# Optimization experiments

Hardware: AMD Instinct MI355X
Metric: run time of the kernel (lower is better)

The kernel has to match this reference:

```python
import jax, jax.numpy as jnp
import numpy as np

N_NODES = 100000
N_EDGES = 3200000
FEATURE = 128
HIDDEN = 128
N_LAYERS = 3


def _glorot(key, fan_in, fan_out):
    lim = np.sqrt(6.0 / (fan_in + fan_out)).astype(np.float32)
    return jax.random.uniform(key, (fan_in, fan_out), jnp.float32, -lim, lim)


def setup_inputs() -> dict:
    key = jax.random.key(0)
    ks = jax.random.split(key, 8)
    x = jax.random.normal(ks[0], (N_NODES, FEATURE), jnp.float32)
    edge_index = jax.random.randint(ks[1], (2, N_EDGES), 0, N_NODES, jnp.int64)
    W0 = _glorot(ks[2], FEATURE, HIDDEN)
    W1 = _glorot(ks[3], HIDDEN, HIDDEN)
    W2 = _glorot(ks[4], HIDDEN, HIDDEN)
    b0 = jnp.zeros((HIDDEN,), jnp.float32)
    b1 = jnp.zeros((HIDDEN,), jnp.float32)
    b2 = jnp.zeros((HIDDEN,), jnp.float32)
    return {"x": x, "edge_index": edge_index,
            "W0": W0, "b0": b0, "W1": W1, "b1": b1, "W2": W2, "b2": b2}


def _gcn_conv(x, W, b, src, dst, n):
    # PyG GCNConv: linear -> add self loops -> sym-norm aggregate -> +bias
    h = x @ W  # [N, H]
    loop = jnp.arange(n)
    s = jnp.concatenate([src, loop])  # sources incl. self loops
    d = jnp.concatenate([dst, loop])  # targets incl. self loops
    deg = jax.ops.segment_sum(jnp.ones_like(d, dtype=h.dtype), d, num_segments=n)
    dinv = jnp.where(deg > 0, jax.lax.rsqrt(jnp.maximum(deg, 1.0)), 0.0)
    norm = dinv[s] * dinv[d]  # [E+N]
    out = jax.ops.segment_sum(h[s] * norm[:, None], d, num_segments=n)
    return out + b


def reference(x, edge_index, W0, b0, W1, b1, W2, b2):
    # forward of GCN: (GCNConv -> relu -> dropout[eval=no-op]) x layer
    src, dst = edge_index[0], edge_index[1]
    n = x.shape[0]
    for W, b in ((W0, b0), (W1, b1), (W2, b2)):
        x = jax.nn.relu(_gcn_conv(x, W, b, src, dst, n))
    return x
```

## Files before the change

kernel.cpp:

```cpp
#include <hip/hip_runtime.h>
#include <hip/hip_fp16.h>

#define N_NODES 100000
#define N_EDGES 3200000
#define NBUCKETS 391
#define CHUNK 12500


__global__ __launch_bounds__(512) void k_bzero(int* __restrict__ bucket_cnt) {
    int t = threadIdx.x;
    if (t < NBUCKETS) bucket_cnt[t] = 0;
}

__global__ __launch_bounds__(256) void k_bhist(const int* __restrict__ ei_dst,
                                               int* __restrict__ bucket_cnt) {
    __shared__ int h[NBUCKETS];
    int t = threadIdx.x;
    for (int i = t; i < NBUCKETS; i += 256) h[i] = 0;
    __syncthreads();
    int base = blockIdx.x * CHUNK;
    for (int i = t; i < CHUNK; i += 256)
        atomicAdd(&h[ei_dst[base + i] >> 8], 1);
    __syncthreads();
    for (int i = t; i < NBUCKETS; i += 256)
        if (h[i]) atomicAdd(&bucket_cnt[i], h[i]);
}

__global__ __launch_bounds__(512) void k_bscan(const int* __restrict__ bucket_cnt,
                                               int* __restrict__ bucket_base,
                                               int* __restrict__ bucket_fill) {
    __shared__ int s[512];
    int t = threadIdx.x;
    int v = (t < NBUCKETS) ? bucket_cnt[t] : 0;
    s[t] = v;
    __syncthreads();
    for (int off = 1; off < 512; off <<= 1) {
        int x = (t >= off) ? s[t - off] : 0;
        __syncthreads();
        s[t] += x;
        __syncthreads();
    }
    int ex = s[t] - v;
    if (t < NBUCKETS) { bucket_base[t] = ex; bucket_fill[t] = ex; }
    if (t == NBUCKETS - 1) bucket_base[NBUCKETS] = s[t];
}

__global__ __launch_bounds__(256) void k_bscatter(const int* __restrict__ ei,
                                                  int* __restrict__ bucket_fill,
                                                  unsigned* __restrict__ bpairs) {
    __shared__ int h[NBUCKETS];
    __shared__ int basep[NBUCKETS];
    int t = threadIdx.x;
    const int* dstp = ei + N_EDGES;
    int base = blockIdx.x * CHUNK;

    for (int i = t; i < NBUCKETS; i += 256) h[i] = 0;
    __syncthreads();
    for (int i = t; i < CHUNK; i += 256)
        atomicAdd(&h[dstp[base + i] >> 8], 1);
    __syncthreads();
    for (int i = t; i < NBUCKETS; i += 256) {
        int c = h[i];
        basep[i] = c ? atomicAdd(&bucket_fill[i], c) : 0;
    }
    __syncthreads();
    for (int i = t; i < NBUCKETS; i += 256) h[i] = 0;
    __syncthreads();
    for (int i = t; i < CHUNK; i += 256) {
        int d = dstp[base + i];
        int s = ei[base + i];
        int b = d >> 8;
        int r = atomicAdd(&h[b], 1);
        bpairs[basep[b] + r] = (unsigned)s | ((unsigned)(d & 255) << 17);
    }
}

__global__ __launch_bounds__(256) void k_bbuild(const unsigned* __restrict__ bpairs,
                                                const int* __restrict__ bucket_base,
                                                int* __restrict__ row_ptr,
                                                int* __restrict__ cnt,
                                                float* __restrict__ dinv,
                                                int* __restrict__ csr_src) {
    __shared__ int h[256];
    __shared__ int sc[256];
    int b = blockIdx.x;
    int t = threadIdx.x;
    int e0 = bucket_base[b], e1 = bucket_base[b + 1];

    h[t] = 0;
    __syncthreads();
    for (int i = e0 + t; i < e1; i += 256)
        atomicAdd(&h[bpairs[i] >> 17], 1);
    __syncthreads();
    int v = h[t];
    sc[t] = v;
    __syncthreads();
    for (int off = 1; off < 256; off <<= 1) {
        int x = (t >= off) ? sc[t - off] : 0;
        __syncthreads();
        sc[t] += x;
        __syncthreads();
    }
    int ex = sc[t] - v;
    int node = b * 256 + t;
    if (node < N_NODES) {
        cnt[node] = v;
        dinv[node] = rsqrtf((float)(v + 1));
        row_ptr[node] = e0 + ex;
    }
    __syncthreads();
    h[t] = e0 + ex;
    __syncthreads();
    for (int i = e0 + t; i < e1; i += 256) {
        unsigned p = bpairs[i];
        int pos = atomicAdd(&h[p >> 17], 1);
        csr_src[pos] = (int)(p & 0x1FFFFu);
    }
}


__global__ __launch_bounds__(256) void k_gemm(const float* __restrict__ X,
                                              const float* __restrict__ W,
                                              const float* __restrict__ dinv,
                                              __half* __restrict__ H16) {
    __shared__ float Ws[64 * 128];
    __shared__ float Xs[64 * 65];

    int t  = threadIdx.x;
    int row0 = blockIdx.x * 64;
    int cg = (t & 15) << 3;
    int rg = (t >> 4) << 2;

    float acc[4][8];
#pragma unroll
    for (int i = 0; i < 4; ++i)
#pragma unroll
        for (int j = 0; j < 8; ++j) acc[i][j] = 0.0f;

    int srow = t >> 4;
    int sk4  = (t & 15) << 2;

    for (int p = 0; p < 2; ++p) {
        __syncthreads();
        const float4* W4 = (const float4*)(W + p * 64 * 128);
        for (int i = t; i < 2048; i += 256) {
            float4 wv = W4[i];
            float* q = &Ws[i << 2];
            q[0] = wv.x; q[1] = wv.y; q[2] = wv.z; q[3] = wv.w;
        }
#pragma unroll
        for (int it = 0; it < 4; ++it) {
            int r = srow + (it << 4);
            int grow = row0 + r;
            if (grow >= N_NODES) grow = N_NODES - 1;
            float4 xv = *(const float4*)(X + (long long)grow * 128 + p * 64 + sk4);
            float* q = &Xs[r * 65 + sk4];
            q[0] = xv.x; q[1] = xv.y; q[2] = xv.z; q[3] = xv.w;
        }
        __syncthreads();
#pragma unroll
        for (int k = 0; k < 64; ++k) {
            const float4 w0 = *(const float4*)&Ws[k * 128 + cg];
            const float4 w1 = *(const float4*)&Ws[k * 128 + cg + 4];
            float x0 = Xs[(rg + 0) * 65 + k];
            float x1 = Xs[(rg + 1) * 65 + k];
            float x2 = Xs[(rg + 2) * 65 + k];
            float x3 = Xs[(rg + 3) * 65 + k];
            acc[0][0] += x0 * w0.x; acc[0][1] += x0 * w0.y; acc[0][2] += x0 * w0.z; acc[0][3] += x0 * w0.w;
            acc[0][4] += x0 * w1.x; acc[0][5] += x0 * w1.y; acc[0][6] += x0 * w1.z; acc[0][7] += x0 * w1.w;
            acc[1][0] += x1 * w0.x; acc[1][1] += x1 * w0.y; acc[1][2] += x1 * w0.z; acc[1][3] += x1 * w0.w;
            acc[1][4] += x1 * w1.x; acc[1][5] += x1 * w1.y; acc[1][6] += x1 * w1.z; acc[1][7] += x1 * w1.w;
            acc[2][0] += x2 * w0.x; acc[2][1] += x2 * w0.y; acc[2][2] += x2 * w0.z; acc[2][3] += x2 * w0.w;
            acc[2][4] += x2 * w1.x; acc[2][5] += x2 * w1.y; acc[2][6] += x2 * w1.z; acc[2][7] += x2 * w1.w;
            acc[3][0] += x3 * w0.x; acc[3][1] += x3 * w0.y; acc[3][2] += x3 * w0.z; acc[3][3] += x3 * w0.w;
            acc[3][4] += x3 * w1.x; acc[3][5] += x3 * w1.y; acc[3][6] += x3 * w1.z; acc[3][7] += x3 * w1.w;
        }
    }

#pragma unroll
    for (int i = 0; i < 4; ++i) {
        int grow = row0 + rg + i;
        if (grow >= N_NODES) break;
        float sc = dinv[grow];
        float4 pack;
        __half2* ph = (__half2*)&pack;
        ph[0] = __floats2half2_rn(acc[i][0] * sc, acc[i][1] * sc);
        ph[1] = __floats2half2_rn(acc[i][2] * sc, acc[i][3] * sc);
        ph[2] = __floats2half2_rn(acc[i][4] * sc, acc[i][5] * sc);
        ph[3] = __floats2half2_rn(acc[i][6] * sc, acc[i][7] * sc);
        *(float4*)(H16 + (long long)grow * 128 + cg) = pack;
    }
}


__global__ __launch_bounds__(256) void k_gather(const __half2* __restrict__ H2,
                                                const int* __restrict__ csr_src,
                                                const int* __restrict__ row_ptr,
                                                const int* __restrict__ cnt,
                                                const float* __restrict__ dinv,
                                                const float* __restrict__ b,
                                                float* __restrict__ out) {
    int node = blockIdx.x * 4 + (threadIdx.x >> 6);
    int lane = threadIdx.x & 63;
    if (node >= N_NODES) return;

    int start = row_ptr[node];
    int n = cnt[node];

    float2 self_ = __half22float2(H2[node * 64 + lane]);
    float accx = self_.x, accy = self_.y;

    int j = 0;
    for (; j + 8 <= n; j += 8) {
        int s[8];
#pragma unroll
        for (int u = 0; u < 8; ++u) s[u] = csr_src[start + j + u];
        float2 h[8];
#pragma unroll
        for (int u = 0; u < 8; ++u) h[u] = __half22float2(H2[s[u] * 64 + lane]);
#pragma unroll
        for (int u = 0; u < 8; ++u) { accx += h[u].x; accy += h[u].y; }
    }
    for (; j < n; ++j) {
        float2 h = __half22float2(H2[csr_src[start + j] * 64 + lane]);
        accx += h.x; accy += h.y;
    }

    float dd = dinv[node];
    float2 bb = ((const float2*)b)[lane];
    float2 v;
    v.x = fmaxf(fmaf(accx, dd, bb.x), 0.0f);
    v.y = fmaxf(fmaf(accy, dd, bb.y), 0.0f);
    ((float2*)out)[node * 64 + lane] = v;
}


extern "C" void kernel_launch(void* const* d_in, const int* in_sizes, int n_in,
                              void* d_out, int out_size, void* d_ws, size_t ws_size,
                              hipStream_t stream) {
    const float* x  = (const float*)d_in[0];
    const int*   ei = (const int*)d_in[1];
    const float* Wm[3] = {(const float*)d_in[2], (const float*)d_in[4], (const float*)d_in[6]};
    const float* bv[3] = {(const float*)d_in[3], (const float*)d_in[5], (const float*)d_in[7]};
    float* out = (float*)d_out;

    char* w = (char*)d_ws;
    int*      row_ptr     = (int*)(w + 0);
    int*      cnt         = (int*)(w + 400384);
    float*    dinv        = (float*)(w + 800768);
    int*      bucket_cnt  = (int*)(w + 1201152);
    int*      bucket_base = (int*)(w + 1203200);
    int*      bucket_fill = (int*)(w + 1205248);
    unsigned* bpairs      = (unsigned*)(w + 1207296);
    int*      csr_src     = (int*)(w + 14007808);
    __half*   H16         = (__half*)(w + 26808320);

    k_bzero<<<1, 512, 0, stream>>>(bucket_cnt);
    k_bhist<<<256, 256, 0, stream>>>(ei + N_EDGES, bucket_cnt);
    k_bscan<<<1, 512, 0, stream>>>(bucket_cnt, bucket_base, bucket_fill);
    k_bscatter<<<256, 256, 0, stream>>>(ei, bucket_fill, bpairs);
    k_bbuild<<<NBUCKETS, 256, 0, stream>>>(bpairs, bucket_base, row_ptr, cnt, dinv, csr_src);

    const float* xin = x;
    for (int l = 0; l < 3; ++l) {
        k_gemm<<<(N_NODES + 63) / 64, 256, 0, stream>>>(xin, Wm[l], dinv, H16);
        k_gather<<<(N_NODES + 3) / 4, 256, 0, stream>>>((const __half2*)H16, csr_src,
                                                        row_ptr, cnt, dinv, bv[l], out);
        xin = out;
    }
}
```

Before: 705.4 us.

## Replace FP32 SIMT GEMM with split-bf16 MFMA GEMM and pre-swizzled weight fragments

Replaces the shared-memory FP32 FMA GEMM with a matrix-core kernel using bf16 16x16x32 MFMA. FP32 accuracy is approximated with a three-term hi/lo split (hi*hi + lo*hi + hi*lo). A new prep kernel converts all three weight matrices once into fragment-ordered bf16 hi/lo arrays. Activations are loaded straight from global memory into registers and split per element, with no LDS staging. The costs are three times the MFMA count plus per-element split arithmetic, and the epilogue now writes scattered 2-byte stores instead of 16-byte vector stores.

New measurement: 650.6 us. 7.8% less time.

```diff
diff --git a/kernel.cpp b/kernel.cpp
--- a/kernel.cpp
+++ b/kernel.cpp
@@ -5,6 +5,19 @@
 #define N_EDGES 3200000
 #define NBUCKETS 391
 #define CHUNK 12500
+
+typedef __attribute__((ext_vector_type(8))) short sh8;
+typedef __attribute__((ext_vector_type(4))) float fl4;
+
+__device__ inline void split_bf16(float x, short& hi, short& lo) {
+    unsigned u = __float_as_uint(x);
+    unsigned r = u + 0x7FFFu + ((u >> 16) & 1u);
+    hi = (short)(r >> 16);
+    float hif = __uint_as_float(r & 0xFFFF0000u);
+    float lof = x - hif;
+    unsigned u2 = __float_as_uint(lof);
+    lo = (short)((u2 + 0x7FFFu + ((u2 >> 16) & 1u)) >> 16);
+}
 
 
 __global__ __launch_bounds__(512) void k_bzero(int* __restrict__ bucket_cnt) {
@@ -119,77 +132,97 @@
 }
 
 
-__global__ __launch_bounds__(256) void k_gemm(const float* __restrict__ X,
-                                              const float* __restrict__ W,
-                                              const float* __restrict__ dinv,
-                                              __half* __restrict__ H16) {
-    __shared__ float Ws[64 * 128];
-    __shared__ float Xs[64 * 65];
-
-    int t  = threadIdx.x;
-    int row0 = blockIdx.x * 64;
-    int cg = (t & 15) << 3;
-    int rg = (t >> 4) << 2;
-
-    float acc[4][8];
-#pragma unroll
-    for (int i = 0; i < 4; ++i)
-#pragma unroll
-        for (int j = 0; j < 8; ++j) acc[i][j] = 0.0f;
-
-    int srow = t >> 4;
-    int sk4  = (t & 15) << 2;
-
-    for (int p = 0; p < 2; ++p) {
-        __syncthreads();
-        const float4* W4 = (const float4*)(W + p * 64 * 128);
-        for (int i = t; i < 2048; i += 256) {
-            float4 wv = W4[i];
-            float* q = &Ws[i << 2];
-            q[0] = wv.x; q[1] = wv.y; q[2] = wv.z; q[3] = wv.w;
+__global__ __launch_bounds__(256) void k_wprep(const float* __restrict__ W0,
+                                               const float* __restrict__ W1,
+                                               const float* __restrict__ W2,
+                                               short* __restrict__ fhi,
+                                               short* __restrict__ flo) {
+    int idx = blockIdx.x * 256 + threadIdx.x;
+    int l = idx >> 14, e = idx & 16383;
+    const float* W = (l == 0) ? W0 : (l == 1) ? W1 : W2;
+    float w = W[e];
+    int k = e >> 7, n = e & 127;
+    int ks = k >> 5, q = (k >> 3) & 3, j = k & 7;
+    int c = n >> 4, n16 = n & 15;
+    int lane = q * 16 + n16;
+    int dst = ((l * 32 + ks * 8 + c) * 64 + lane) * 8 + j;
+    short hi, lo;
+    split_bf16(w, hi, lo);
+    fhi[dst] = hi;
+    flo[dst] = lo;
+}
+
+
+__global__ __launch_bounds__(256) void k_gemm_mfma(const float* __restrict__ X,
+                                                   const short* __restrict__ fhi,
+                                                   const short* __restrict__ flo,
+                                                   const float* __restrict__ dinv,
+                                                   __half* __restrict__ H16,
+                                                   int layer) {
+    int t = threadIdx.x;
+    int wave = t >> 6, lane = t & 63;
+    int q = lane >> 4, n16 = lane & 15;
+    int row_base = blockIdx.x * 128 + wave * 32;
+
+    const sh8* __restrict__ BH = (const sh8*)(fhi + layer * 16384);
+    const sh8* __restrict__ BL = (const sh8*)(flo + layer * 16384);
+
+    fl4 acc[2][8];
+#pragma unroll
+    for (int r = 0; r < 2; ++r)
+#pragma unroll
+        for (int c = 0; c < 8; ++c) acc[r][c] = (fl4){0.f, 0.f, 0.f, 0.f};
+
+    long long arow[2];
+    {
+        int r0 = row_base + n16;       if (r0 > N_NODES - 1) r0 = N_NODES - 1;
+        int r1 = row_base + 16 + n16;  if (r1 > N_NODES - 1) r1 = N_NODES - 1;
+        arow[0] = r0; arow[1] = r1;
+    }
+
+#pragma unroll
+    for (int ks = 0; ks < 4; ++ks) {
+        sh8 ah[2], al[2];
+#pragma unroll
+        for (int r = 0; r < 2; ++r) {
+            const float* px = X + arow[r] * 128 + ks * 32 + q * 8;
+            float4 x0 = *(const float4*)px;
+            float4 x1 = *(const float4*)(px + 4);
+            float xs[8] = {x0.x, x0.y, x0.z, x0.w, x1.x, x1.y, x1.z, x1.w};
+#pragma unroll
+            for (int j = 0; j < 8; ++j) {
+                short h, l;
+                split_bf16(xs[j], h, l);
+                ah[r][j] = h;
+                al[r][j] = l;
+            }
         }
 #pragma unroll
-        for (int it = 0; it < 4; ++it) {
-            int r = srow + (it << 4);
-            int grow = row0 + r;
-            if (grow >= N_NODES) grow = N_NODES - 1;
-            float4 xv = *(const float4*)(X + (long long)grow * 128 + p * 64 + sk4);
-            float* q = &Xs[r * 65 + sk4];
-            q[0] = xv.x; q[1] = xv.y; q[2] = xv.z; q[3] = xv.w;
+        for (int c = 0; c < 8; ++c) {
+            sh8 bh = BH[(ks * 8 + c) * 64 + lane];
+            sh8 bl = BL[(ks * 8 + c) * 64 + lane];
+#pragma unroll
+            for (int r = 0; r < 2; ++r) {
+                acc[r][c] = __builtin_amdgcn_mfma_f32_16x16x32_bf16(ah[r], bh, acc[r][c], 0, 0, 0);
+                acc[r][c] = __builtin_amdgcn_mfma_f32_16x16x32_bf16(al[r], bh, acc[r][c], 0, 0, 0);
+                acc[r][c] = __builtin_amdgcn_mfma_f32_16x16x32_bf16(ah[r], bl, acc[r][c], 0, 0, 0);
+            }
         }
-        __syncthreads();
-#pragma unroll
-        for (int k = 0; k < 64; ++k) {
-            const float4 w0 = *(const float4*)&Ws[k * 128 + cg];
-            const float4 w1 = *(const float4*)&Ws[k * 128 + cg + 4];
-            float x0 = Xs[(rg + 0) * 65 + k];
-            float x1 = Xs[(rg + 1) * 65 + k];
-            float x2 = Xs[(rg + 2) * 65 + k];
-            float x3 = Xs[(rg + 3) * 65 + k];
-            acc[0][0] += x0 * w0.x; acc[0][1] += x0 * w0.y; acc[0][2] += x0 * w0.z; acc[0][3] += x0 * w0.w;
-            acc[0][4] += x0 * w1.x; acc[0][5] += x0 * w1.y; acc[0][6] += x0 * w1.z; acc[0][7] += x0 * w1.w;
-            acc[1][0] += x1 * w0.x; acc[1][1] += x1 * w0.y; acc[1][2] += x1 * w0.z; acc[1][3] += x1 * w0.w;
-            acc[1][4] += x1 * w1.x; acc[1][5] += x1 * w1.y; acc[1][6] += x1 * w1.z; acc[1][7] += x1 * w1.w;
-            acc[2][0] += x2 * w0.x; acc[2][1] += x2 * w0.y; acc[2][2] += x2 * w0.z; acc[2][3] += x2 * w0.w;
-            acc[2][4] += x2 * w1.x; acc[2][5] += x2 * w1.y; acc[2][6] += x2 * w1.z; acc[2][7] += x2 * w1.w;
-            acc[3][0] += x3 * w0.x; acc[3][1] += x3 * w0.y; acc[3][2] += x3 * w0.z; acc[3][3] += x3 * w0.w;
-            acc[3][4] += x3 * w1.x; acc[3][5] += x3 * w1.y; acc[3][6] += x3 * w1.z; acc[3][7] += x3 * w1.w;
+    }
+
+#pragma unroll
+    for (int r = 0; r < 2; ++r)
+#pragma unroll
+        for (int reg = 0; reg < 4; ++reg) {
+            int grow = row_base + r * 16 + q * 4 + reg;
+            if (grow < N_NODES) {
+                float sc = dinv[grow];
+                __half* dst = H16 + (long long)grow * 128 + n16;
+#pragma unroll
+                for (int c = 0; c < 8; ++c)
+                    dst[c * 16] = __float2half(acc[r][c][reg] * sc);
+            }
         }
-    }
-
-#pragma unroll
-    for (int i = 0; i < 4; ++i) {
-        int grow = row0 + rg + i;
-        if (grow >= N_NODES) break;
-        float sc = dinv[grow];
-        float4 pack;
-        __half2* ph = (__half2*)&pack;
-        ph[0] = __floats2half2_rn(acc[i][0] * sc, acc[i][1] * sc);
-        ph[1] = __floats2half2_rn(acc[i][2] * sc, acc[i][3] * sc);
-        ph[2] = __floats2half2_rn(acc[i][4] * sc, acc[i][5] * sc);
-        ph[3] = __floats2half2_rn(acc[i][6] * sc, acc[i][7] * sc);
-        *(float4*)(H16 + (long long)grow * 128 + cg) = pack;
-    }
 }
 
 
@@ -253,17 +286,21 @@
     int*      bucket_fill = (int*)(w + 1205248);
     unsigned* bpairs      = (unsigned*)(w + 1207296);
     int*      csr_src     = (int*)(w + 14007808);
-    __half*   H16         = (__half*)(w + 26808320);
+    short*    fragHi      = (short*)(w + 26808320);
+    short*    fragLo      = (short*)(w + 26906624);
+    __half*   H16         = (__half*)(w + 27004928);
 
     k_bzero<<<1, 512, 0, stream>>>(bucket_cnt);
     k_bhist<<<256, 256, 0, stream>>>(ei + N_EDGES, bucket_cnt);
     k_bscan<<<1, 512, 0, stream>>>(bucket_cnt, bucket_base, bucket_fill);
     k_bscatter<<<256, 256, 0, stream>>>(ei, bucket_fill, bpairs);
     k_bbuild<<<NBUCKETS, 256, 0, stream>>>(bpairs, bucket_base, row_ptr, cnt, dinv, csr_src);
+    k_wprep<<<192, 256, 0, stream>>>(Wm[0], Wm[1], Wm[2], fragHi, fragLo);
 
     const float* xin = x;
     for (int l = 0; l < 3; ++l) {
-        k_gemm<<<(N_NODES + 63) / 64, 256, 0, stream>>>(xin, Wm[l], dinv, H16);
+        k_gemm_mfma<<<(N_NODES + 127) / 128, 256, 0, stream>>>(xin, fragHi, fragLo,
+                                                               dinv, H16, l);
         k_gather<<<(N_NODES + 3) / 4, 256, 0, stream>>>((const __half2*)H16, csr_src,
                                                         row_ptr, cnt, dinv, bv[l], out);
         xin = out;
```
